# Optimization experiments

Measured on AMD Instinct MI355X. Metric: run time of the kernel, lower is better.

## Reference

```python
import jax, jax.numpy as jnp
import numpy as np

STRIDE = 1
PAD = 1

def setup_inputs() -> dict:
    key = jax.random.key(0)
    k1, k2 = jax.random.split(key)
    x = jax.random.normal(k1, (32, 128, 56, 56), dtype=jnp.float32)
    weight = jax.random.normal(k2, (256, 128, 3, 3), dtype=jnp.float32) * 0.1
    b = jnp.zeros((256,), dtype=jnp.float32)
    return {"x": x, "weight": weight, "b": b}

def reference(x, weight, b):
    # Binarize weights with sign (matches torch.sign: sign(0)=0), then plain conv2d.
    bw = jnp.sign(weight)
    out = jax.lax.conv_general_dilated(
        x, bw,
        window_strides=(STRIDE, STRIDE),
        padding=((PAD, PAD), (PAD, PAD)),
        dimension_numbers=("NCHW", "OIHW", "NCHW"),
    )
    return out + b[None, :, None, None]
```

## Files before the change

### kernel.cpp

```cpp
#include <hip/hip_runtime.h>
#include <hip/hip_bf16.h>

typedef __attribute__((ext_vector_type(8))) short bf16x8;
typedef __attribute__((ext_vector_type(4))) float f32x4;

#define CIN   128
#define COUT  256
#define NIMG  32
#define HWDIM 56
#define HPAD  58
#define KTOT  1152
#define HWIMG 3136
#define MTOT  100352
#define BS    128
#define BF    128
#define BK    64

__device__ __forceinline__ void gload16(const void* g, void* l) {
  __builtin_amdgcn_global_load_lds((const __attribute__((address_space(1))) void*)g,
                                   (__attribute__((address_space(3))) void*)l,
                                   16, 0, 0);
}

__global__ __launch_bounds__(256)
void zero_xp(float4* __restrict__ p, int n16) {
  int i = blockIdx.x * 256 + threadIdx.x;
  int stride = gridDim.x * 256;
  float4 z; z.x = 0.f; z.y = 0.f; z.z = 0.f; z.w = 0.f;
  for (; i < n16; i += stride) p[i] = z;
}

__global__ __launch_bounds__(256)
void prep_x(const float* __restrict__ x, __hip_bfloat16* __restrict__ xp) {
  __shared__ float tile[CIN * 57];
  const int nh = blockIdx.x;
  const int n = nh / HWDIM;
  const int h = nh - n * HWDIM;
  const int t = threadIdx.x;

  const float* src = x + (size_t)n * CIN * HWIMG + (size_t)h * HWDIM;
  for (int i = t; i < CIN * HWDIM; i += 256) {
    int c = i / HWDIM;
    int w = i - c * HWDIM;
    tile[c * 57 + w] = src[(size_t)c * HWIMG + w];
  }
  __syncthreads();

  __hip_bfloat16* dst = xp + (((size_t)n * HPAD + (h + 1)) * HPAD + 1) * CIN;
  for (int o = t; o < HWDIM * 64; o += 256) {
    int w = o >> 6;
    int c = (o & 63) * 2;
    __hip_bfloat162 pr;
    pr.x = __float2bfloat16(tile[c * 57 + w]);
    pr.y = __float2bfloat16(tile[(c + 1) * 57 + w]);
    *reinterpret_cast<__hip_bfloat162*>(dst + (size_t)w * CIN + c) = pr;
  }
}

__global__ __launch_bounds__(256)
void prep_w(const float* __restrict__ wsrc, __hip_bfloat16* __restrict__ wt) {
  int o = blockIdx.x * 256 + threadIdx.x;
  if (o >= COUT * KTOT) return;
  int cout = o / KTOT;
  int r = o - cout * KTOT;
  int tap = r >> 7;
  int cin = r & 127;
  float v = wsrc[((size_t)cout * CIN + cin) * 9 + tap];
  float s = (v > 0.f) ? 1.f : ((v < 0.f) ? -1.f : 0.f);
  wt[o] = __float2bfloat16(s);
}

__global__ __launch_bounds__(256, 2)
void bconv_mfma(const short* __restrict__ xp, const short* __restrict__ wt,
                const float* __restrict__ bias, float* __restrict__ out) {
  __shared__ short lw[BF * BK];
  __shared__ short lx[BS * BK];

  const int tid  = threadIdx.x;
  const int lane = tid & 63;
  const int wv   = tid >> 6;
  const int wm   = wv >> 1;
  const int wn   = wv & 1;
  const int s0   = blockIdx.x * BS;
  const int f0   = blockIdx.y * BF;

  const int srow = tid >> 3;
  const int slot = tid & 7;
  const int swz  = slot ^ (srow & 7);

  int xoff[4];
  int woff[4];
#pragma unroll
  for (int r = 0; r < 4; ++r) {
    int m  = s0 + r * 32 + srow;
    int n  = m / HWIMG;
    int hw = m - n * HWIMG;
    int h  = hw / HWDIM;
    int w  = hw - h * HWDIM;
    xoff[r] = ((n * HPAD + h) * HPAD + w) * CIN + swz * 8;
    woff[r] = (f0 + r * 32 + srow) * KTOT + swz * 8;
  }

  f32x4 acc[4][4] = {};

  short* lwdst = &lw[(wv * 8) * BK];
  short* lxdst = &lx[(wv * 8) * BK];

  for (int ks = 0; ks < 18; ++ks) {
    const int tap = ks >> 1;
    const int kh  = tap / 3;
    const int kw  = tap - kh * 3;
    const int xko = (kh * HPAD + kw) * CIN + (ks & 1) * BK;
    const int wko = ks * BK;

    __syncthreads();
#pragma unroll
    for (int r = 0; r < 4; ++r) {
      gload16(wt + woff[r] + wko, lwdst + r * 32 * BK);
      gload16(xp + xoff[r] + xko, lxdst + r * 32 * BK);
    }
    __syncthreads();

#pragma unroll
    for (int ksub = 0; ksub < 2; ++ksub) {
      const int rlo = lane & 15;
      const int sx  = (ksub * 4 + (lane >> 4)) ^ (rlo & 7);
      bf16x8 af[4], bx[4];
#pragma unroll
      for (int f = 0; f < 4; ++f) {
        int row = wm * 64 + f * 16 + rlo;
        af[f] = *(const bf16x8*)&lw[row * BK + sx * 8];
      }
#pragma unroll
      for (int f = 0; f < 4; ++f) {
        int row = wn * 64 + f * 16 + rlo;
        bx[f] = *(const bf16x8*)&lx[row * BK + sx * 8];
      }
#pragma unroll
      for (int fm = 0; fm < 4; ++fm)
#pragma unroll
        for (int fn = 0; fn < 4; ++fn)
          acc[fm][fn] = __builtin_amdgcn_mfma_f32_16x16x32_bf16(
              af[fm], bx[fn], acc[fm][fn], 0, 0, 0);
    }
  }

  const int col = lane & 15;
  const int rg  = lane >> 4;
#pragma unroll
  for (int fn = 0; fn < 4; ++fn) {
    int m  = s0 + wn * 64 + fn * 16 + col;
    int n  = m / HWIMG;
    int hw = m - n * HWIMG;
    float* obase = out + (size_t)n * (COUT * HWIMG) + hw;
#pragma unroll
    for (int fm = 0; fm < 4; ++fm) {
      int c0 = f0 + wm * 64 + fm * 16 + rg * 4;
#pragma unroll
      for (int j = 0; j < 4; ++j) {
        int c = c0 + j;
        obase[(size_t)c * HWIMG] = acc[fm][fn][j] + bias[c];
      }
    }
  }
}

extern "C" void kernel_launch(void* const* d_in, const int* in_sizes, int n_in,
                              void* d_out, int out_size, void* d_ws, size_t ws_size,
                              hipStream_t stream) {
  const float* x  = (const float*)d_in[0];
  const float* w  = (const float*)d_in[1];
  const float* b  = (const float*)d_in[2];
  float* out = (float*)d_out;

  const size_t xp_elems = (size_t)NIMG * HPAD * HPAD * CIN;
  __hip_bfloat16* xp = (__hip_bfloat16*)d_ws;
  __hip_bfloat16* wt = xp + xp_elems;

  int n16 = (int)(xp_elems / 8);
  zero_xp<<<2048, 256, 0, stream>>>((float4*)d_ws, n16);

  prep_x<<<NIMG * HWDIM, 256, 0, stream>>>(x, xp);

  prep_w<<<(COUT * KTOT + 255) / 256, 256, 0, stream>>>(w, wt);

  dim3 grid(MTOT / BS, COUT / BF);
  bconv_mfma<<<grid, 256, 0, stream>>>((const short*)xp, (const short*)wt, b, out);
}
```

Baseline: 103.4 us.

## Rewrite conv GEMM as 256x256-tile 8-wave kernel with triple-buffered LDS pipeline

```diff
diff --git a/kernel.cpp b/kernel.cpp
--- a/kernel.cpp
+++ b/kernel.cpp
@@ -12,9 +12,9 @@
 #define KTOT  1152
 #define HWIMG 3136
 #define MTOT  100352
-#define BS    128
-#define BF    128
-#define BK    64
+#define BN    256
+#define BK    32
+#define NT    36
 
 __device__ __forceinline__ void gload16(const void* g, void* l) {
   __builtin_amdgcn_global_load_lds((const __attribute__((address_space(1))) void*)g,
@@ -23,11 +23,26 @@
 }
 
 __global__ __launch_bounds__(256)
-void zero_xp(float4* __restrict__ p, int n16) {
-  int i = blockIdx.x * 256 + threadIdx.x;
-  int stride = gridDim.x * 256;
-  float4 z; z.x = 0.f; z.y = 0.f; z.z = 0.f; z.w = 0.f;
-  for (; i < n16; i += stride) p[i] = z;
+void zero_halo(__hip_bfloat16* __restrict__ xp) {
+  int idx = blockIdx.x * 256 + threadIdx.x;
+  int n = idx / 3648;
+  int r = idx - n * 3648;
+  size_t base = (size_t)n * HPAD * HPAD * CIN;
+  size_t off;
+  if (r < 1856) {
+    int half = r / 928;
+    int c = r - half * 928;
+    off = base + (size_t)(half ? 57 : 0) * HPAD * CIN + (size_t)c * 8;
+  } else {
+    int r2 = r - 1856;
+    int h = 1 + (r2 >> 5);
+    int rem = r2 & 31;
+    int side = rem >> 4;
+    int chunk = rem & 15;
+    off = base + ((size_t)h * HPAD + (side ? 57 : 0)) * CIN + (size_t)chunk * 8;
+  }
+  int4 z; z.x = 0; z.y = 0; z.z = 0; z.w = 0;
+  *reinterpret_cast<int4*>(xp + off) = z;
 }
 
 __global__ __launch_bounds__(256)
@@ -70,120 +85,147 @@
   wt[o] = __float2bfloat16(s);
 }
 
-__global__ __launch_bounds__(256, 2)
-void bconv_mfma(const short* __restrict__ xp, const short* __restrict__ wt,
-                const float* __restrict__ bias, float* __restrict__ out) {
-  __shared__ short lw[BF * BK];
-  __shared__ short lx[BS * BK];
+__global__ __launch_bounds__(512, 2)
+void bconv8(const short* __restrict__ xp, const short* __restrict__ wt,
+            const float* __restrict__ bias, float* __restrict__ out) {
+  __shared__ short lw[3][COUT * BK];
+  __shared__ short lx[3][BN * BK];
 
   const int tid  = threadIdx.x;
   const int lane = tid & 63;
   const int wv   = tid >> 6;
-  const int wm   = wv >> 1;
-  const int wn   = wv & 1;
-  const int s0   = blockIdx.x * BS;
-  const int f0   = blockIdx.y * BF;
-
-  const int srow = tid >> 3;
-  const int slot = tid & 7;
-  const int swz  = slot ^ (srow & 7);
-
-  int xoff[4];
-  int woff[4];
-#pragma unroll
-  for (int r = 0; r < 4; ++r) {
-    int m  = s0 + r * 32 + srow;
+  const int wm   = wv >> 2;
+  const int wn   = wv & 3;
+  const int s0   = blockIdx.x * BN;
+
+  const int srow = tid >> 2;
+  const int slot = tid & 3;
+
+  int xbase[2];
+#pragma unroll
+  for (int r = 0; r < 2; ++r) {
+    int m  = s0 + r * 128 + srow;
     int n  = m / HWIMG;
     int hw = m - n * HWIMG;
     int h  = hw / HWDIM;
     int w  = hw - h * HWDIM;
-    xoff[r] = ((n * HPAD + h) * HPAD + w) * CIN + swz * 8;
-    woff[r] = (f0 + r * 32 + srow) * KTOT + swz * 8;
-  }
-
-  f32x4 acc[4][4] = {};
-
-  short* lwdst = &lw[(wv * 8) * BK];
-  short* lxdst = &lx[(wv * 8) * BK];
-
-  for (int ks = 0; ks < 18; ++ks) {
-    const int tap = ks >> 1;
-    const int kh  = tap / 3;
-    const int kw  = tap - kh * 3;
-    const int xko = (kh * HPAD + kw) * CIN + (ks & 1) * BK;
-    const int wko = ks * BK;
-
-    __syncthreads();
-#pragma unroll
-    for (int r = 0; r < 4; ++r) {
-      gload16(wt + woff[r] + wko, lwdst + r * 32 * BK);
-      gload16(xp + xoff[r] + xko, lxdst + r * 32 * BK);
+    xbase[r] = ((n * HPAD + h) * HPAD + w) * CIN + slot * 8;
+  }
+  const int wbase = srow * KTOT + slot * 8;
+
+#define LWDST(S, R) ((short*)&lw[(S)][((R) * 128 + wv * 16) * BK])
+#define LXDST(S, R) ((short*)&lx[(S)][((R) * 128 + wv * 16) * BK])
+#define XKO(T) (((((T) >> 2) / 3) * HPAD + (((T) >> 2) - (((T) >> 2) / 3) * 3)) * CIN + ((T) & 3) * 32)
+
+  f32x4 acc[8][4] = {};
+
+#pragma unroll
+  for (int r = 0; r < 2; ++r) gload16(wt + r * 128 * KTOT + wbase + 0 * BK, LWDST(0, r));
+#pragma unroll
+  for (int r = 0; r < 2; ++r) gload16(xp + xbase[r] + XKO(0), LXDST(0, r));
+#pragma unroll
+  for (int r = 0; r < 2; ++r) gload16(wt + r * 128 * KTOT + wbase + 1 * BK, LWDST(1, r));
+#pragma unroll
+  for (int r = 0; r < 2; ++r) gload16(xp + xbase[r] + XKO(1), LXDST(1, r));
+  asm volatile("s_waitcnt vmcnt(4)" ::: "memory");
+  __builtin_amdgcn_s_barrier();
+
+  const int rlo = lane & 15;
+  const int kq  = lane >> 4;
+
+  int s = 0;
+  for (int t = 0; t < NT; ++t) {
+    int s2 = s + 2; if (s2 >= 3) s2 -= 3;
+    const short* A = &lw[s][0];
+    const short* B = &lx[s][0];
+
+    bf16x8 af[4], bx[4];
+#pragma unroll
+    for (int f = 0; f < 4; ++f)
+      af[f] = *(const bf16x8*)&A[(wm * 128 + f * 16 + rlo) * BK + kq * 8];
+#pragma unroll
+    for (int f = 0; f < 4; ++f)
+      bx[f] = *(const bf16x8*)&B[(wn * 64 + f * 16 + rlo) * BK + kq * 8];
+    if (t + 2 < NT) {
+      const int ko = (t + 2) * BK;
+#pragma unroll
+      for (int r = 0; r < 2; ++r) gload16(wt + r * 128 * KTOT + wbase + ko, LWDST(s2, r));
     }
-    __syncthreads();
-
-#pragma unroll
-    for (int ksub = 0; ksub < 2; ++ksub) {
-      const int rlo = lane & 15;
-      const int sx  = (ksub * 4 + (lane >> 4)) ^ (rlo & 7);
-      bf16x8 af[4], bx[4];
-#pragma unroll
-      for (int f = 0; f < 4; ++f) {
-        int row = wm * 64 + f * 16 + rlo;
-        af[f] = *(const bf16x8*)&lw[row * BK + sx * 8];
-      }
-#pragma unroll
-      for (int f = 0; f < 4; ++f) {
-        int row = wn * 64 + f * 16 + rlo;
-        bx[f] = *(const bf16x8*)&lx[row * BK + sx * 8];
-      }
-#pragma unroll
-      for (int fm = 0; fm < 4; ++fm)
-#pragma unroll
-        for (int fn = 0; fn < 4; ++fn)
-          acc[fm][fn] = __builtin_amdgcn_mfma_f32_16x16x32_bf16(
-              af[fm], bx[fn], acc[fm][fn], 0, 0, 0);
+    __builtin_amdgcn_s_barrier();
+    asm volatile("s_waitcnt lgkmcnt(0)" ::: "memory");
+    __builtin_amdgcn_sched_barrier(0);
+    __builtin_amdgcn_s_setprio(1);
+#pragma unroll
+    for (int mf = 0; mf < 4; ++mf)
+#pragma unroll
+      for (int nf = 0; nf < 4; ++nf)
+        acc[mf][nf] = __builtin_amdgcn_mfma_f32_16x16x32_bf16(af[mf], bx[nf], acc[mf][nf], 0, 0, 0);
+    __builtin_amdgcn_s_setprio(0);
+    __builtin_amdgcn_s_barrier();
+
+#pragma unroll
+    for (int f = 0; f < 4; ++f)
+      af[f] = *(const bf16x8*)&A[(wm * 128 + 64 + f * 16 + rlo) * BK + kq * 8];
+    if (t + 2 < NT) {
+      const int xko = XKO(t + 2);
+#pragma unroll
+      for (int r = 0; r < 2; ++r) gload16(xp + xbase[r] + xko, LXDST(s2, r));
     }
+    if (t + 2 < NT) asm volatile("s_waitcnt vmcnt(4)" ::: "memory");
+    else            asm volatile("s_waitcnt vmcnt(0)" ::: "memory");
+    __builtin_amdgcn_s_barrier();
+    asm volatile("s_waitcnt lgkmcnt(0)" ::: "memory");
+    __builtin_amdgcn_sched_barrier(0);
+    __builtin_amdgcn_s_setprio(1);
+#pragma unroll
+    for (int mf = 0; mf < 4; ++mf)
+#pragma unroll
+      for (int nf = 0; nf < 4; ++nf)
+        acc[4 + mf][nf] = __builtin_amdgcn_mfma_f32_16x16x32_bf16(af[mf], bx[nf], acc[4 + mf][nf], 0, 0, 0);
+    __builtin_amdgcn_s_setprio(0);
+    __builtin_amdgcn_s_barrier();
+
+    s = s + 1; if (s == 3) s = 0;
   }
 
   const int col = lane & 15;
   const int rg  = lane >> 4;
 #pragma unroll
-  for (int fn = 0; fn < 4; ++fn) {
-    int m  = s0 + wn * 64 + fn * 16 + col;
+  for (int nf = 0; nf < 4; ++nf) {
+    int m  = s0 + wn * 64 + nf * 16 + col;
     int n  = m / HWIMG;
     int hw = m - n * HWIMG;
-    float* obase = out + (size_t)n * (COUT * HWIMG) + hw;
-#pragma unroll
-    for (int fm = 0; fm < 4; ++fm) {
-      int c0 = f0 + wm * 64 + fm * 16 + rg * 4;
-#pragma unroll
-      for (int j = 0; j < 4; ++j) {
-        int c = c0 + j;
-        obase[(size_t)c * HWIMG] = acc[fm][fn][j] + bias[c];
-      }
+    float* ob = out + (size_t)n * (COUT * HWIMG) + hw;
+#pragma unroll
+    for (int mf = 0; mf < 8; ++mf) {
+      int c0 = wm * 128 + mf * 16 + rg * 4;
+      const float4 bv = *reinterpret_cast<const float4*>(&bias[c0]);
+      ob[(size_t)(c0 + 0) * HWIMG] = acc[mf][nf][0] + bv.x;
+      ob[(size_t)(c0 + 1) * HWIMG] = acc[mf][nf][1] + bv.y;
+      ob[(size_t)(c0 + 2) * HWIMG] = acc[mf][nf][2] + bv.z;
+      ob[(size_t)(c0 + 3) * HWIMG] = acc[mf][nf][3] + bv.w;
     }
   }
+#undef LWDST
+#undef LXDST
+#undef XKO
 }
 
 extern "C" void kernel_launch(void* const* d_in, const int* in_sizes, int n_in,
                               void* d_out, int out_size, void* d_ws, size_t ws_size,
                               hipStream_t stream) {
-  const float* x  = (const float*)d_in[0];
-  const float* w  = (const float*)d_in[1];
-  const float* b  = (const float*)d_in[2];
+  const float* x = (const float*)d_in[0];
+  const float* w = (const float*)d_in[1];
+  const float* b = (const float*)d_in[2];
   float* out = (float*)d_out;
 
   const size_t xp_elems = (size_t)NIMG * HPAD * HPAD * CIN;
   __hip_bfloat16* xp = (__hip_bfloat16*)d_ws;
   __hip_bfloat16* wt = xp + xp_elems;
 
-  int n16 = (int)(xp_elems / 8);
-  zero_xp<<<2048, 256, 0, stream>>>((float4*)d_ws, n16);
-
+  zero_halo<<<456, 256, 0, stream>>>(xp);
   prep_x<<<NIMG * HWDIM, 256, 0, stream>>>(x, xp);
-
   prep_w<<<(COUT * KTOT + 255) / 256, 256, 0, stream>>>(w, wt);
 
-  dim3 grid(MTOT / BS, COUT / BF);
-  bconv_mfma<<<grid, 256, 0, stream>>>((const short*)xp, (const short*)wt, b, out);
-}
+  bconv8<<<MTOT / BN, 512, 0, stream>>>((const short*)xp, (const short*)wt, b, out);
+}
```

Result: slower. 117.6 us (+13.8%).
